# Kernel tuning notes

Measured on AMD Instinct MI355X. Metric: run time of the kernel, lower is better.

Reference implementation:

```python
import jax, jax.numpy as jnp
import numpy as np

B, N, T, D = 64, 76, 128, 128
AH, HEADS, DFF, FAH = 8, 4, 512, 128
DK = D // HEADS


def layer_norm(x, a, b, eps=1e-7):
    mean = x.mean(-1, keepdims=True)
    std = jnp.std(x, -1, ddof=1, keepdims=True)  # torch.std is unbiased
    return a * (x - mean) / (std + eps) + b


def setup_inputs() -> dict:
    key = jax.random.key(0)
    ks = jax.random.split(key, 32)
    w = lambda i, shape, s=0.05: (jax.random.normal(ks[i], shape, jnp.float32) * s)
    return {
        "H": jax.random.normal(ks[0], (B, N, T, D), jnp.float32),
        "mask": jax.random.randint(ks[1], (B, N, T), 0, 2).astype(jnp.float32),
        "feature_mask": jax.random.uniform(ks[2], (B, N), dtype=jnp.float32),
        # MissingAwareTemporalAttention params (shared across features)
        "Wt": w(3, (D, AH), 0.1), "Wx": w(4, (D, AH), 0.1),
        "rate": jnp.array([0.8], jnp.float32),
        "obs_bias": jnp.float32(0.5), "miss_bias": jnp.float32(0.0),
        # MultiHeadedAttention params (weights stored [in,out])
        "Wq": w(5, (D, D)), "bq": jnp.zeros(D, jnp.float32),
        "Wk": w(6, (D, D)), "bk": jnp.zeros(D, jnp.float32),
        "Wv": w(7, (D, D)), "bv": jnp.zeros(D, jnp.float32),
        "Wo": w(8, (D, D)), "bo": jnp.zeros(D, jnp.float32),
        # SublayerConnection LayerNorms
        "ln1_a": jnp.ones(D, jnp.float32), "ln1_b": jnp.zeros(D, jnp.float32),
        "ln2_a": jnp.ones(D, jnp.float32), "ln2_b": jnp.zeros(D, jnp.float32),
        # PositionwiseFeedForward
        "w1": w(9, (D, DFF)), "b1": jnp.zeros(DFF, jnp.float32),
        "w2": w(10, (DFF, D)), "b2": jnp.zeros(D, jnp.float32),
        # FinalAttentionQKV ('mul')
        "fWq": w(11, (D, FAH)), "fbq": jnp.zeros(FAH, jnp.float32),
        "fWk": w(12, (D, FAH)), "fbk": jnp.zeros(FAH, jnp.float32),
        "fWv": w(13, (D, FAH)), "fbv": jnp.zeros(FAH, jnp.float32),
        "mask_scale": jnp.float32(1.0),
    }


def concare_forward(H, mask, feature_mask, Wt, Wx, rate, obs_bias, miss_bias,
                    Wq, bq, Wk, bk, Wv, bv, Wo, bo, ln1_a, ln1_b, ln2_a, ln2_b,
                    w1, b1, w2, b2, fWq, fbq, fWk, fbk, fWv, fbv, mask_scale):
    # ---- MissingAwareTemporalAttention per feature (vectorized over N) ----
    q = jnp.einsum('bnd,da->bna', H[:, :, -1, :], Wt)           # [B,N,AH]
    k = jnp.einsum('bntd,da->bnta', H, Wx)                      # [B,N,T,AH]
    dot = jnp.einsum('bna,bnta->bnt', q, k)                     # [B,N,T]
    b_time = (jnp.arange(T - 1, -1, -1, dtype=jnp.float32) + 1.0)  # [T]
    sig = jax.nn.sigmoid(dot)
    denom = jax.nn.sigmoid(rate[0]) * (jnp.log(2.72 + (1.0 - sig)) * b_time)
    e = jax.nn.relu(sig / denom)
    e = e + jnp.where(mask > 0.5, obs_bias, miss_bias)
    a = jax.nn.softmax(e, axis=-1)                              # over T
    emb = jnp.einsum('bnt,bntd->bnd', a, H)                     # [B,N,D]

    # ---- SublayerConnection 1: pre-norm + MultiHeadedAttention + residual ----
    x0 = layer_norm(emb, ln1_a, ln1_b)
    qh = (x0 @ Wq + bq).reshape(B, N, HEADS, DK).transpose(0, 2, 1, 3)
    kh = (x0 @ Wk + bk).reshape(B, N, HEADS, DK).transpose(0, 2, 1, 3)
    vh = (x0 @ Wv + bv).reshape(B, N, HEADS, DK).transpose(0, 2, 1, 3)
    scores = jnp.einsum('bhqd,bhkd->bhqk', qh, kh) / np.sqrt(DK)
    p = jax.nn.softmax(scores, axis=-1)
    ctx = jnp.einsum('bhqk,bhkd->bhqd', p, vh).transpose(0, 2, 1, 3).reshape(B, N, D)
    mha = ctx @ Wo + bo                                          # [B,N,D]
    # DeCov regularizer over batch, per feature position
    feats = jnp.transpose(mha, (1, 2, 0))                        # [N,D,B]
    centered = feats - feats.mean(axis=2, keepdims=True)
    cov = jnp.einsum('ndb,neb->nde', centered, centered) / (B - 1)
    diag = jnp.einsum('ndd->nd', cov)
    decov = 0.5 * (jnp.sum(cov ** 2) - jnp.sum(diag ** 2))
    x = emb + mha

    # ---- SublayerConnection 2: pre-norm + FFN + residual ----
    x1 = layer_norm(x, ln2_a, ln2_b)
    ffn = jax.nn.relu(x1 @ w1 + b1) @ w2 + b2
    x = x + ffn                                                  # [B,N,D]

    # ---- FinalAttentionQKV ('mul') ----
    fq = x[:, -1, :] @ fWq + fbq                                 # [B,FAH]
    fk = x @ fWk + fbk                                           # [B,N,FAH]
    fv = x @ fWv + fbv                                           # [B,N,FAH]
    fe = jnp.einsum('bna,ba->bn', fk, fq)
    fe = fe + mask_scale * feature_mask
    alpha = jax.nn.softmax(fe, axis=1)                           # over N
    pooled = jnp.einsum('bn,bna->ba', alpha, fv)                 # [B,FAH]
    return pooled, decov


def reference(H, mask, feature_mask, Wt, Wx, rate, obs_bias, miss_bias,
              Wq, bq, Wk, bk, Wv, bv, Wo, bo, ln1_a, ln1_b, ln2_a, ln2_b,
              w1, b1, w2, b2, fWq, fbq, fWk, fbk, fWv, fbv, mask_scale):
    return concare_forward(H, mask, feature_mask, Wt, Wx, rate, obs_bias, miss_bias,
                           Wq, bq, Wk, bk, Wv, bv, Wo, bo, ln1_a, ln1_b, ln2_a, ln2_b,
                           w1, b1, w2, b2, fWq, fbq, fWk, fbk, fWv, fbv, mask_scale)
```

## Files before the change

kernel.cpp:

```cpp
#include <hip/hip_runtime.h>
#include <hip/hip_bf16.h>
#include <math.h>

#define BB 64
#define NN 76
#define TT 128
#define DD 128
#define AH 8
#define NHEADS 4
#define DFF 512
#define FAH 128
#define DK 32
#define BN (BB*NN)
#define ROWS 8
#define NBLK (BN/ROWS)

__device__ __forceinline__ void bar_lds() {
    asm volatile("s_waitcnt lgkmcnt(0)" ::: "memory");
    __builtin_amdgcn_s_barrier();
    __builtin_amdgcn_sched_barrier(0);
}

__global__ __launch_bounds__(512, 8) void k1_temporal(
    const float* __restrict__ H, const float* __restrict__ mask,
    const float* __restrict__ Wt, const float* __restrict__ Wx,
    const float* __restrict__ rate, const float* __restrict__ obs_bias,
    const float* __restrict__ miss_bias, float* __restrict__ emb)
{
    __shared__ __align__(16) float wtx[2*DD*AH];
    __shared__ __align__(16) float wqs[DD];
    __shared__ __align__(16) float dots[TT];
    __shared__ __align__(16) float as_[TT];
    __shared__ __align__(16) float parts[16][DD];
    __shared__ float qpart[2][AH];
    __shared__ float redsum[2];

    const int bid = blockIdx.x;
    const int tid = threadIdx.x;
    const size_t base = (size_t)bid * (TT*DD);
    const int lane = tid & 63, w = tid >> 6;
    const int c = tid & 31, g = tid >> 5;

    const float* wsrc = (tid < 256) ? (Wt + 4*tid) : (Wx + 4*(tid-256));
    const float4 wld = *(const float4*)wsrc;
    float r127 = 0.f, maskv = 0.f;
    if (tid < DD) {
        r127  = H[base + (TT-1)*DD + tid];
        maskv = mask[(size_t)bid*TT + tid];
    }
    const float sr   = 1.f / (1.f + expf(-rate[0]));
    const float obsv = obs_bias[0], missv = miss_bias[0];

    float4 h[8];
    const float4* Hg4 = (const float4*)(H + base);
    #pragma unroll
    for (int j = 0; j < 8; ++j) h[j] = Hg4[j*512 + tid];

    *(float4*)&wtx[4*tid] = wld;
    bar_lds();

    if (tid < DD) {
        float p[AH];
        #pragma unroll
        for (int a = 0; a < AH; ++a) p[a] = r127 * wtx[tid*AH + a];
        #pragma unroll
        for (int a = 0; a < AH; ++a) {
            float v = p[a];
            #pragma unroll
            for (int m = 1; m < 64; m <<= 1) v += __shfl_xor(v, m, 64);
            if (lane == 0) qpart[w][a] = v;
        }
    }
    bar_lds();
    if (tid < DD) {
        float acc = 0.f;
        #pragma unroll
        for (int a = 0; a < AH; ++a)
            acc += (qpart[0][a] + qpart[1][a]) * wtx[DD*AH + tid*AH + a];
        wqs[tid] = acc;
    }
    bar_lds();

    const float4 wq4 = *(const float4*)&wqs[4*c];
    #pragma unroll
    for (int j = 0; j < 8; ++j) {
        float p = h[j].x*wq4.x + h[j].y*wq4.y + h[j].z*wq4.z + h[j].w*wq4.w;
        #pragma unroll
        for (int m = 1; m < 32; m <<= 1) p += __shfl_xor(p, m, 64);
        if (c == 0) dots[g + 16*j] = p;
    }
    bar_lds();

    if (tid < TT) {
        const float dot = dots[tid];
        const float sig = 1.f / (1.f + expf(-dot));
        const float bt  = (float)(TT - tid);
        const float denom = sr * (logf(2.72f + (1.f - sig)) * bt);
        float e = fmaxf(sig / denom, 0.f);
        e += (maskv > 0.5f) ? obsv : missv;
        const float ex = expf(e);
        as_[tid] = ex;
        float vs = ex;
        #pragma unroll
        for (int m = 1; m < 64; m <<= 1) vs += __shfl_xor(vs, m, 64);
        if (lane == 0) redsum[w] = vs;
    }
    bar_lds();
    const float inv = 1.f / (redsum[0] + redsum[1]);

    float4 facc = make_float4(0.f, 0.f, 0.f, 0.f);
    #pragma unroll
    for (int j = 0; j < 8; ++j) {
        const float a = as_[g + 16*j];
        facc.x += a*h[j].x; facc.y += a*h[j].y;
        facc.z += a*h[j].z; facc.w += a*h[j].w;
    }
    *(float4*)&parts[g][4*c] = facc;
    bar_lds();
    if (tid < DD) {
        float acc = 0.f;
        #pragma unroll
        for (int gg = 0; gg < 16; ++gg) acc += parts[gg][tid];
        emb[(size_t)bid*DD + tid] = acc * inv;
    }
}

__global__ __launch_bounds__(256) void k2a_ln_qkv(
    const float* __restrict__ emb,
    const float* __restrict__ ln_a, const float* __restrict__ ln_b,
    const float* __restrict__ Wq, const float* __restrict__ bq,
    const float* __restrict__ Wk, const float* __restrict__ bk,
    const float* __restrict__ Wv, const float* __restrict__ bv,
    float* __restrict__ qb, float* __restrict__ kb, float* __restrict__ vb)
{
    __shared__ float xs[ROWS][DD];
    const int tid = threadIdx.x;
    const int r0 = blockIdx.x * ROWS;

    for (int i = tid; i < ROWS*DD; i += 256) {
        const int r = i / DD, d = i % DD;
        xs[r][d] = emb[(size_t)(r0+r)*DD + d];
    }
    __syncthreads();

    {
        const int wv_ = tid >> 6, lane = tid & 63;
        for (int rr = 0; rr < 2; ++rr) {
            const int r = wv_*2 + rr;
            const float x0 = xs[r][lane], x1 = xs[r][lane+64];
            float s = x0 + x1;
            #pragma unroll
            for (int m = 1; m < 64; m <<= 1) s += __shfl_xor(s, m, 64);
            const float mean = s / (float)DD;
            const float d0 = x0 - mean, d1 = x1 - mean;
            float v = d0*d0 + d1*d1;
            #pragma unroll
            for (int m = 1; m < 64; m <<= 1) v += __shfl_xor(v, m, 64);
            const float inv = 1.f / (sqrtf(v / (float)(DD-1)) + 1e-7f);
            xs[r][lane]    = ln_a[lane]   * (d0*inv) + ln_b[lane];
            xs[r][lane+64] = ln_a[lane+64]* (d1*inv) + ln_b[lane+64];
        }
    }
    __syncthreads();

    const int j = tid & 127, half = tid >> 7, rbase = half*4;
    float aq[4] = {0,0,0,0}, ak[4] = {0,0,0,0}, av[4] = {0,0,0,0};
    for (int d = 0; d < DD; ++d) {
        const float wqv = Wq[d*DD+j], wkv = Wk[d*DD+j], wvv = Wv[d*DD+j];
        #pragma unroll
        for (int r = 0; r < 4; ++r) {
            const float xv = xs[rbase+r][d];
            aq[r] += xv*wqv; ak[r] += xv*wkv; av[r] += xv*wvv;
        }
    }
    const float bqv = bq[j], bkv = bk[j], bvv = bv[j];
    #pragma unroll
    for (int r = 0; r < 4; ++r) {
        const size_t o = (size_t)(r0 + rbase + r)*DD + j;
        qb[o] = aq[r]+bqv; kb[o] = ak[r]+bkv; vb[o] = av[r]+bvv;
    }
}

__global__ __launch_bounds__(128) void k2b_attn(
    const float* __restrict__ qb, const float* __restrict__ kb,
    const float* __restrict__ vb, float* __restrict__ ctx)
{
    __shared__ float Qs[NN][DK], Ks[NN][DK], Vs[NN][DK];
    __shared__ float Ps[NN][NN+1];
    const int b = blockIdx.x / NHEADS, h = blockIdx.x % NHEADS;
    const int tid = threadIdx.x;
    const int co = h*DK;

    for (int i = tid; i < NN*DK; i += 128) {
        const int r = i / DK, c = i % DK;
        const size_t o = (size_t)(b*NN + r)*DD + co + c;
        Qs[r][c] = qb[o]; Ks[r][c] = kb[o]; Vs[r][c] = vb[o];
    }
    __syncthreads();

    const float scale = 0.17677669529663687f;
    if (tid < NN) {
        float qr[DK];
        #pragma unroll
        for (int c = 0; c < DK; ++c) qr[c] = Qs[tid][c];
        float mx = -1e30f;
        for (int k = 0; k < NN; ++k) {
            float s = 0.f;
            #pragma unroll
            for (int c = 0; c < DK; ++c) s += qr[c]*Ks[k][c];
            s *= scale;
            Ps[tid][k] = s;
            mx = fmaxf(mx, s);
        }
        float sum = 0.f;
        for (int k = 0; k < NN; ++k) { const float e = expf(Ps[tid][k]-mx); Ps[tid][k] = e; sum += e; }
        const float inv = 1.f/sum;
        float acc[DK];
        #pragma unroll
        for (int c = 0; c < DK; ++c) acc[c] = 0.f;
        for (int k = 0; k < NN; ++k) {
            const float p = Ps[tid][k];
            #pragma unroll
            for (int c = 0; c < DK; ++c) acc[c] += p*Vs[k][c];
        }
        const size_t o = (size_t)(b*NN + tid)*DD + co;
        #pragma unroll
        for (int c = 0; c < DK; ++c) ctx[o+c] = acc[c]*inv;
    }
}

__global__ __launch_bounds__(256) void k23_proj_ffn(
    const float* __restrict__ ctx, const float* __restrict__ emb,
    const float* __restrict__ Wo, const float* __restrict__ bo,
    const float* __restrict__ ln_a, const float* __restrict__ ln_b,
    const float* __restrict__ w1, const float* __restrict__ b1,
    const float* __restrict__ w2, const float* __restrict__ b2,
    float* __restrict__ mha, float* __restrict__ x2)
{
    __shared__ float cs[ROWS][DD];
    __shared__ float xs[ROWS][DD];
    __shared__ float x1s[ROWS][DD];
    __shared__ float hs[ROWS][DFF];
    __shared__ float parts[2][ROWS][DD];
    const int tid = threadIdx.x;
    const int r0 = blockIdx.x * ROWS;

    for (int i = tid; i < ROWS*DD; i += 256) {
        const int r = i / DD, d = i % DD;
        cs[r][d] = ctx[(size_t)(r0+r)*DD + d];
    }
    __syncthreads();

    {
        const int j = tid & 127, half = tid >> 7, rbase = half*4;
        float acc[4] = {0,0,0,0};
        for (int d = 0; d < DD; ++d) {
            const float wv = Wo[d*DD+j];
            #pragma unroll
            for (int r = 0; r < 4; ++r) acc[r] += cs[rbase+r][d]*wv;
        }
        const float bov = bo[j];
        #pragma unroll
        for (int r = 0; r < 4; ++r) {
            const size_t o = (size_t)(r0+rbase+r)*DD + j;
            const float m = acc[r] + bov;
            mha[o] = m;
            xs[rbase+r][j] = emb[o] + m;
        }
    }
    __syncthreads();

    {
        const int wv_ = tid >> 6, lane = tid & 63;
        for (int rr = 0; rr < 2; ++rr) {
            const int r = wv_*2 + rr;
            const float v0 = xs[r][lane], v1 = xs[r][lane+64];
            float s = v0 + v1;
            #pragma unroll
            for (int m = 1; m < 64; m <<= 1) s += __shfl_xor(s, m, 64);
            const float mean = s / (float)DD;
            const float d0 = v0-mean, d1 = v1-mean;
            float vv = d0*d0 + d1*d1;
            #pragma unroll
            for (int m = 1; m < 64; m <<= 1) vv += __shfl_xor(vv, m, 64);
            const float inv = 1.f / (sqrtf(vv/(float)(DD-1)) + 1e-7f);
            x1s[r][lane]    = ln_a[lane]   * (d0*inv) + ln_b[lane];
            x1s[r][lane+64] = ln_a[lane+64]* (d1*inv) + ln_b[lane+64];
        }
    }
    __syncthreads();

    {
        float acc0[ROWS], acc1[ROWS];
        #pragma unroll
        for (int r = 0; r < ROWS; ++r) { acc0[r]=0.f; acc1[r]=0.f; }
        for (int d = 0; d < DD; ++d) {
            const float wv0 = w1[d*DFF + tid], wv1 = w1[d*DFF + tid + 256];
            #pragma unroll
            for (int r = 0; r < ROWS; ++r) {
                const float xv = x1s[r][d];
                acc0[r] += xv*wv0; acc1[r] += xv*wv1;
            }
        }
        const float b10 = b1[tid], b11 = b1[tid+256];
        #pragma unroll
        for (int r = 0; r < ROWS; ++r) {
            hs[r][tid]     = fmaxf(acc0[r]+b10, 0.f);
            hs[r][tid+256] = fmaxf(acc1[r]+b11, 0.f);
        }
    }
    __syncthreads();

    {
        const int j = tid & 127, half = tid >> 7;
        float acc[ROWS];
        #pragma unroll
        for (int r = 0; r < ROWS; ++r) acc[r] = 0.f;
        for (int k = half*256; k < half*256 + 256; ++k) {
            const float wv = w2[k*DD + j];
            #pragma unroll
            for (int r = 0; r < ROWS; ++r) acc[r] += hs[r][k]*wv;
        }
        #pragma unroll
        for (int r = 0; r < ROWS; ++r) parts[half][r][j] = acc[r];
        __syncthreads();
        if (half == 0) {
            const float b2v = b2[j];
            #pragma unroll
            for (int r = 0; r < ROWS; ++r) {
                const size_t o = (size_t)(r0+r)*DD + j;
                x2[o] = xs[r][j] + parts[0][r][j] + parts[1][r][j] + b2v;
            }
        }
    }
}

__global__ __launch_bounds__(256) void k_decov(
    const float* __restrict__ mha, float* __restrict__ partial)
{
    __shared__ float Cs[BB][DD];
    __shared__ float means[DD];
    __shared__ float reda[256];
    __shared__ float redb[256];
    const int n = blockIdx.x, dc = blockIdx.y;
    const int tid = threadIdx.x;
    for (int i = tid; i < BB*DD; i += 256) {
        const int bb = i / DD, d = i % DD;
        Cs[bb][d] = mha[((size_t)bb*NN + n)*DD + d];
    }
    __syncthreads();
    if (tid < DD) {
        float s = 0.f;
        for (int bb = 0; bb < BB; ++bb) s += Cs[bb][tid];
        means[tid] = s / (float)BB;
    }
    __syncthreads();
    if (tid < DD) {
        const float m = means[tid];
        for (int bb = 0; bb < BB; ++bb) Cs[bb][tid] -= m;
    }
    __syncthreads();
    float ss = 0.f, dd2 = 0.f;
    const float invB1 = 1.f/63.f;
    for (int qi = tid; qi < 1024; qi += 256) {
        const int d  = dc*32 + qi / 32;
        const int e4 = (qi % 32) * 4;
        float a0=0,a1=0,a2=0,a3=0;
        for (int bb = 0; bb < BB; ++bb) {
            const float cd = Cs[bb][d];
            const float4 ce = *(const float4*)&Cs[bb][e4];
            a0 += cd*ce.x; a1 += cd*ce.y; a2 += cd*ce.z; a3 += cd*ce.w;
        }
        a0*=invB1; a1*=invB1; a2*=invB1; a3*=invB1;
        ss += a0*a0+a1*a1+a2*a2+a3*a3;
        if (d >= e4 && d < e4+4) {
            const float c[4] = {a0,a1,a2,a3};
            const float cd = c[d-e4];
            dd2 += cd*cd;
        }
    }
    reda[tid] = ss; redb[tid] = dd2;
    __syncthreads();
    for (int s2 = 128; s2 >= 1; s2 >>= 1) {
        if (tid < s2) { reda[tid] += reda[tid+s2]; redb[tid] += redb[tid+s2]; }
        __syncthreads();
    }
    if (tid == 0) partial[n*4 + dc] = 0.5f*(reda[0] - redb[0]);
}

__global__ __launch_bounds__(128) void k4_final(
    const float* __restrict__ x, const float* __restrict__ feature_mask,
    const float* __restrict__ fWq, const float* __restrict__ fbq,
    const float* __restrict__ fWk, const float* __restrict__ fbk,
    const float* __restrict__ fWv, const float* __restrict__ fbv,
    const float* __restrict__ mask_scale, const float* __restrict__ decov_partial,
    float* __restrict__ out)
{
    __shared__ float Xs[NN][DD];
    __shared__ float fqs[DD], gs[DD], ys[DD];
    __shared__ float es[NN];
    __shared__ float sc[2];
    const int b = blockIdx.x;
    const int tid = threadIdx.x;
    for (int i = tid; i < NN*DD; i += 128) {
        const int r = i / DD, d = i % DD;
        Xs[r][d] = x[((size_t)b*NN + r)*DD + d];
    }
    __syncthreads();
    {
        float acc = 0.f;
        for (int d = 0; d < DD; ++d) acc += Xs[NN-1][d] * fWq[d*FAH + tid];
        fqs[tid] = acc + fbq[tid];
    }
    __syncthreads();
    {
        float acc = 0.f;
        for (int a = 0; a < FAH; ++a) acc += fWk[tid*FAH + a] * fqs[a];
        gs[tid] = acc;
    }
    if (tid == 0) {
        float acc = 0.f;
        for (int a = 0; a < FAH; ++a) acc += fbk[a]*fqs[a];
        sc[0] = acc;
    }
    __syncthreads();
    const float msc = mask_scale[0];
    if (tid < NN) {
        float acc = 0.f;
        for (int d = 0; d < DD; ++d) acc += Xs[tid][d]*gs[d];
        es[tid] = acc + sc[0] + msc * feature_mask[b*NN + tid];
    }
    __syncthreads();
    if (tid == 0) {
        float mx = -1e30f;
        for (int n2 = 0; n2 < NN; ++n2) mx = fmaxf(mx, es[n2]);
        float sum = 0.f;
        for (int n2 = 0; n2 < NN; ++n2) { const float e = expf(es[n2]-mx); es[n2] = e; sum += e; }
        sc[1] = 1.f/sum;
    }
    __syncthreads();
    {
        const float inv = sc[1];
        float acc = 0.f;
        for (int n2 = 0; n2 < NN; ++n2) acc += es[n2]*Xs[n2][tid];
        ys[tid] = acc * inv;
    }
    __syncthreads();
    {
        float acc = 0.f;
        for (int d = 0; d < DD; ++d) acc += ys[d]*fWv[d*FAH + tid];
        out[(size_t)b*FAH + tid] = acc + fbv[tid];
    }
    if (b == 0 && tid == 0) {
        float s = 0.f;
        for (int i = 0; i < NN*4; ++i) s += decov_partial[i];
        out[BB*FAH] = s;
    }
}

extern "C" void kernel_launch(void* const* d_in, const int* in_sizes, int n_in,
                              void* d_out, int out_size, void* d_ws, size_t ws_size,
                              hipStream_t stream) {
    const float* H    = (const float*)d_in[0];
    const float* mask = (const float*)d_in[1];
    const float* fm   = (const float*)d_in[2];
    const float* Wt   = (const float*)d_in[3];
    const float* Wx   = (const float*)d_in[4];
    const float* rate = (const float*)d_in[5];
    const float* obs_bias  = (const float*)d_in[6];
    const float* miss_bias = (const float*)d_in[7];
    const float* Wq = (const float*)d_in[8];   const float* bq = (const float*)d_in[9];
    const float* Wk = (const float*)d_in[10];  const float* bk = (const float*)d_in[11];
    const float* Wv = (const float*)d_in[12];  const float* bv = (const float*)d_in[13];
    const float* Wo = (const float*)d_in[14];  const float* bo = (const float*)d_in[15];
    const float* ln1a = (const float*)d_in[16]; const float* ln1b = (const float*)d_in[17];
    const float* ln2a = (const float*)d_in[18]; const float* ln2b = (const float*)d_in[19];
    const float* w1 = (const float*)d_in[20];  const float* b1 = (const float*)d_in[21];
    const float* w2 = (const float*)d_in[22];  const float* b2 = (const float*)d_in[23];
    const float* fWq = (const float*)d_in[24]; const float* fbq = (const float*)d_in[25];
    const float* fWk = (const float*)d_in[26]; const float* fbk = (const float*)d_in[27];
    const float* fWv = (const float*)d_in[28]; const float* fbv = (const float*)d_in[29];
    const float* mask_scale = (const float*)d_in[30];
    float* out = (float*)d_out;

    float* ws = (float*)d_ws;
    const size_t S = (size_t)BN*DD;
    float* emb = ws;
    float* qb  = ws + 1*S;
    float* kb  = ws + 2*S;
    float* vb  = ws + 3*S;
    float* ctx = ws + 4*S;
    float* mha = ws + 5*S;
    float* x2  = ws + 6*S;
    float* dpart = ws + 7*S;

    k1_temporal<<<BN, 512, 0, stream>>>(H, mask, Wt, Wx, rate, obs_bias, miss_bias, emb);
    k2a_ln_qkv<<<NBLK, 256, 0, stream>>>(emb, ln1a, ln1b, Wq, bq, Wk, bk, Wv, bv, qb, kb, vb);
    k2b_attn<<<BB*NHEADS, 128, 0, stream>>>(qb, kb, vb, ctx);
    k23_proj_ffn<<<NBLK, 256, 0, stream>>>(ctx, emb, Wo, bo, ln2a, ln2b, w1, b1, w2, b2, mha, x2);
    k_decov<<<dim3(NN, 4), 256, 0, stream>>>(mha, dpart);
    k4_final<<<BB, 128, 0, stream>>>(x2, fm, fWq, fbq, fWk, fbk, fWv, fbv, mask_scale, dpart, out);
}
```

Baseline: 181.5 us.

## Double rows per block and merge decov and final attention into one launch

ROWS goes from 8 to 16 in the LN+QKV and projection+FFN kernels, so each block reuses every weight load across twice as many rows, at the cost of half as many blocks and more registers and LDS. The decov kernel and the final-attention kernel are merged into a single launch that branches on block index. Decov partials are now summed with atomicAdd into the output, which the projection kernel zeroes first. This removes one kernel launch and the serial partial-sum loop, but makes the floating-point summation order nondeterministic.

```diff
diff --git a/kernel.cpp b/kernel.cpp
--- a/kernel.cpp
+++ b/kernel.cpp
@@ -12,7 +12,7 @@
 #define FAH 128
 #define DK 32
 #define BN (BB*NN)
-#define ROWS 8
+#define ROWS 16
 #define NBLK (BN/ROWS)
 
 __device__ __forceinline__ void bar_lds() {
@@ -145,8 +145,8 @@
 
     {
         const int wv_ = tid >> 6, lane = tid & 63;
-        for (int rr = 0; rr < 2; ++rr) {
-            const int r = wv_*2 + rr;
+        for (int rr = 0; rr < 4; ++rr) {
+            const int r = wv_*4 + rr;
             const float x0 = xs[r][lane], x1 = xs[r][lane+64];
             float s = x0 + x1;
             #pragma unroll
@@ -163,19 +163,19 @@
     }
     __syncthreads();
 
-    const int j = tid & 127, half = tid >> 7, rbase = half*4;
-    float aq[4] = {0,0,0,0}, ak[4] = {0,0,0,0}, av[4] = {0,0,0,0};
+    const int j = tid & 127, half = tid >> 7, rbase = half*8;
+    float aq[8] = {0}, ak[8] = {0}, av[8] = {0};
     for (int d = 0; d < DD; ++d) {
         const float wqv = Wq[d*DD+j], wkv = Wk[d*DD+j], wvv = Wv[d*DD+j];
         #pragma unroll
-        for (int r = 0; r < 4; ++r) {
+        for (int r = 0; r < 8; ++r) {
             const float xv = xs[rbase+r][d];
             aq[r] += xv*wqv; ak[r] += xv*wkv; av[r] += xv*wvv;
         }
     }
     const float bqv = bq[j], bkv = bk[j], bvv = bv[j];
     #pragma unroll
-    for (int r = 0; r < 4; ++r) {
+    for (int r = 0; r < 8; ++r) {
         const size_t o = (size_t)(r0 + rbase + r)*DD + j;
         qb[o] = aq[r]+bqv; kb[o] = ak[r]+bkv; vb[o] = av[r]+bvv;
     }
@@ -235,7 +235,7 @@
     const float* __restrict__ ln_a, const float* __restrict__ ln_b,
     const float* __restrict__ w1, const float* __restrict__ b1,
     const float* __restrict__ w2, const float* __restrict__ b2,
-    float* __restrict__ mha, float* __restrict__ x2)
+    float* __restrict__ mha, float* __restrict__ x2, float* __restrict__ out)
 {
     __shared__ float cs[ROWS][DD];
     __shared__ float xs[ROWS][DD];
@@ -245,6 +245,8 @@
     const int tid = threadIdx.x;
     const int r0 = blockIdx.x * ROWS;
 
+    if (blockIdx.x == 0 && tid == 0) out[BB*FAH] = 0.f;
+
     for (int i = tid; i < ROWS*DD; i += 256) {
         const int r = i / DD, d = i % DD;
         cs[r][d] = ctx[(size_t)(r0+r)*DD + d];
@@ -252,16 +254,16 @@
     __syncthreads();
 
     {
-        const int j = tid & 127, half = tid >> 7, rbase = half*4;
-        float acc[4] = {0,0,0,0};
+        const int j = tid & 127, half = tid >> 7, rbase = half*8;
+        float acc[8] = {0};
         for (int d = 0; d < DD; ++d) {
             const float wv = Wo[d*DD+j];
             #pragma unroll
-            for (int r = 0; r < 4; ++r) acc[r] += cs[rbase+r][d]*wv;
+            for (int r = 0; r < 8; ++r) acc[r] += cs[rbase+r][d]*wv;
         }
         const float bov = bo[j];
         #pragma unroll
-        for (int r = 0; r < 4; ++r) {
+        for (int r = 0; r < 8; ++r) {
             const size_t o = (size_t)(r0+rbase+r)*DD + j;
             const float m = acc[r] + bov;
             mha[o] = m;
@@ -272,8 +274,8 @@
 
     {
         const int wv_ = tid >> 6, lane = tid & 63;
-        for (int rr = 0; rr < 2; ++rr) {
-            const int r = wv_*2 + rr;
+        for (int rr = 0; rr < 4; ++rr) {
+            const int r = wv_*4 + rr;
             const float v0 = xs[r][lane], v1 = xs[r][lane+64];
             float s = v0 + v1;
             #pragma unroll
@@ -335,85 +337,84 @@
     }
 }
 
-__global__ __launch_bounds__(256) void k_decov(
-    const float* __restrict__ mha, float* __restrict__ partial)
-{
-    __shared__ float Cs[BB][DD];
-    __shared__ float means[DD];
-    __shared__ float reda[256];
-    __shared__ float redb[256];
-    const int n = blockIdx.x, dc = blockIdx.y;
-    const int tid = threadIdx.x;
-    for (int i = tid; i < BB*DD; i += 256) {
-        const int bb = i / DD, d = i % DD;
-        Cs[bb][d] = mha[((size_t)bb*NN + n)*DD + d];
-    }
-    __syncthreads();
-    if (tid < DD) {
-        float s = 0.f;
-        for (int bb = 0; bb < BB; ++bb) s += Cs[bb][tid];
-        means[tid] = s / (float)BB;
-    }
-    __syncthreads();
-    if (tid < DD) {
-        const float m = means[tid];
-        for (int bb = 0; bb < BB; ++bb) Cs[bb][tid] -= m;
-    }
-    __syncthreads();
-    float ss = 0.f, dd2 = 0.f;
-    const float invB1 = 1.f/63.f;
-    for (int qi = tid; qi < 1024; qi += 256) {
-        const int d  = dc*32 + qi / 32;
-        const int e4 = (qi % 32) * 4;
-        float a0=0,a1=0,a2=0,a3=0;
-        for (int bb = 0; bb < BB; ++bb) {
-            const float cd = Cs[bb][d];
-            const float4 ce = *(const float4*)&Cs[bb][e4];
-            a0 += cd*ce.x; a1 += cd*ce.y; a2 += cd*ce.z; a3 += cd*ce.w;
-        }
-        a0*=invB1; a1*=invB1; a2*=invB1; a3*=invB1;
-        ss += a0*a0+a1*a1+a2*a2+a3*a3;
-        if (d >= e4 && d < e4+4) {
-            const float c[4] = {a0,a1,a2,a3};
-            const float cd = c[d-e4];
-            dd2 += cd*cd;
-        }
-    }
-    reda[tid] = ss; redb[tid] = dd2;
-    __syncthreads();
-    for (int s2 = 128; s2 >= 1; s2 >>= 1) {
-        if (tid < s2) { reda[tid] += reda[tid+s2]; redb[tid] += redb[tid+s2]; }
-        __syncthreads();
-    }
-    if (tid == 0) partial[n*4 + dc] = 0.5f*(reda[0] - redb[0]);
-}
-
-__global__ __launch_bounds__(128) void k4_final(
-    const float* __restrict__ x, const float* __restrict__ feature_mask,
+__global__ __launch_bounds__(256) void k_final(
+    const float* __restrict__ mha, const float* __restrict__ x,
+    const float* __restrict__ feature_mask,
     const float* __restrict__ fWq, const float* __restrict__ fbq,
     const float* __restrict__ fWk, const float* __restrict__ fbk,
     const float* __restrict__ fWv, const float* __restrict__ fbv,
-    const float* __restrict__ mask_scale, const float* __restrict__ decov_partial,
-    float* __restrict__ out)
+    const float* __restrict__ mask_scale, float* __restrict__ out)
 {
+    const int tid = threadIdx.x;
+
+    if (blockIdx.x < NN*4) {
+        __shared__ float Cs[BB][DD];
+        __shared__ float means[DD];
+        __shared__ float reda[256];
+        __shared__ float redb[256];
+        const int n = blockIdx.x >> 2, dc = blockIdx.x & 3;
+        for (int i = tid; i < BB*DD; i += 256) {
+            const int bb = i / DD, d = i % DD;
+            Cs[bb][d] = mha[((size_t)bb*NN + n)*DD + d];
+        }
+        __syncthreads();
+        if (tid < DD) {
+            float s = 0.f;
+            for (int bb = 0; bb < BB; ++bb) s += Cs[bb][tid];
+            means[tid] = s / (float)BB;
+        }
+        __syncthreads();
+        if (tid < DD) {
+            const float m = means[tid];
+            for (int bb = 0; bb < BB; ++bb) Cs[bb][tid] -= m;
+        }
+        __syncthreads();
+        float ss = 0.f, dd2 = 0.f;
+        const float invB1 = 1.f/63.f;
+        for (int qi = tid; qi < 1024; qi += 256) {
+            const int d  = dc*32 + qi / 32;
+            const int e4 = (qi % 32) * 4;
+            float a0=0,a1=0,a2=0,a3=0;
+            for (int bb = 0; bb < BB; ++bb) {
+                const float cd = Cs[bb][d];
+                const float4 ce = *(const float4*)&Cs[bb][e4];
+                a0 += cd*ce.x; a1 += cd*ce.y; a2 += cd*ce.z; a3 += cd*ce.w;
+            }
+            a0*=invB1; a1*=invB1; a2*=invB1; a3*=invB1;
+            ss += a0*a0+a1*a1+a2*a2+a3*a3;
+            if (d >= e4 && d < e4+4) {
+                const float c[4] = {a0,a1,a2,a3};
+                const float cd = c[d-e4];
+                dd2 += cd*cd;
+            }
+        }
+        reda[tid] = ss; redb[tid] = dd2;
+        __syncthreads();
+        for (int s2 = 128; s2 >= 1; s2 >>= 1) {
+            if (tid < s2) { reda[tid] += reda[tid+s2]; redb[tid] += redb[tid+s2]; }
+            __syncthreads();
+        }
+        if (tid == 0) atomicAdd(&out[BB*FAH], 0.5f*(reda[0] - redb[0]));
+        return;
+    }
+
     __shared__ float Xs[NN][DD];
     __shared__ float fqs[DD], gs[DD], ys[DD];
     __shared__ float es[NN];
     __shared__ float sc[2];
-    const int b = blockIdx.x;
-    const int tid = threadIdx.x;
-    for (int i = tid; i < NN*DD; i += 128) {
+    const int b = blockIdx.x - NN*4;
+    for (int i = tid; i < NN*DD; i += 256) {
         const int r = i / DD, d = i % DD;
         Xs[r][d] = x[((size_t)b*NN + r)*DD + d];
     }
     __syncthreads();
-    {
+    if (tid < FAH) {
         float acc = 0.f;
         for (int d = 0; d < DD; ++d) acc += Xs[NN-1][d] * fWq[d*FAH + tid];
         fqs[tid] = acc + fbq[tid];
     }
     __syncthreads();
-    {
+    if (tid < DD) {
         float acc = 0.f;
         for (int a = 0; a < FAH; ++a) acc += fWk[tid*FAH + a] * fqs[a];
         gs[tid] = acc;
@@ -439,22 +440,17 @@
         sc[1] = 1.f/sum;
     }
     __syncthreads();
-    {
+    if (tid < DD) {
         const float inv = sc[1];
         float acc = 0.f;
         for (int n2 = 0; n2 < NN; ++n2) acc += es[n2]*Xs[n2][tid];
         ys[tid] = acc * inv;
     }
     __syncthreads();
-    {
+    if (tid < FAH) {
         float acc = 0.f;
         for (int d = 0; d < DD; ++d) acc += ys[d]*fWv[d*FAH + tid];
         out[(size_t)b*FAH + tid] = acc + fbv[tid];
-    }
-    if (b == 0 && tid == 0) {
-        float s = 0.f;
-        for (int i = 0; i < NN*4; ++i) s += decov_partial[i];
-        out[BB*FAH] = s;
     }
 }
 
@@ -492,12 +488,10 @@
     float* ctx = ws + 4*S;
     float* mha = ws + 5*S;
     float* x2  = ws + 6*S;
-    float* dpart = ws + 7*S;
 
     k1_temporal<<<BN, 512, 0, stream>>>(H, mask, Wt, Wx, rate, obs_bias, miss_bias, emb);
     k2a_ln_qkv<<<NBLK, 256, 0, stream>>>(emb, ln1a, ln1b, Wq, bq, Wk, bk, Wv, bv, qb, kb, vb);
     k2b_attn<<<BB*NHEADS, 128, 0, stream>>>(qb, kb, vb, ctx);
-    k23_proj_ffn<<<NBLK, 256, 0, stream>>>(ctx, emb, Wo, bo, ln2a, ln2b, w1, b1, w2, b2, mha, x2);
-    k_decov<<<dim3(NN, 4), 256, 0, stream>>>(mha, dpart);
-    k4_final<<<BB, 128, 0, stream>>>(x2, fm, fWq, fbq, fWk, fbk, fWv, fbv, mask_scale, dpart, out);
-}
+    k23_proj_ffn<<<NBLK, 256, 0, stream>>>(ctx, emb, Wo, bo, ln2a, ln2b, w1, b1, w2, b2, mha, x2, out);
+    k_final<<<NN*4 + BB, 256, 0, stream>>>(mha, x2, fm, fWq, fbq, fWk, fbk, fWv, fbv, mask_scale, out);
+}
```

After: 225.2 us. 24.1% more time.

## Compute query projection and softmax redundantly per wave to cut block barriers

Applied to the files above, without the earlier changes.

The temporal attention kernel now has every wave compute the query projection and the attention softmax weights itself, using shuffles and padded LDS weight layouts, instead of a few threads computing them and sharing through shared memory. This removes three block-wide barriers and the shared-memory staging of intermediate values. In exchange each wave repeats the same transcendental and reduction work, and the occupancy hint in launch bounds drops from 8 to 6.

```diff
diff --git a/kernel.cpp b/kernel.cpp
--- a/kernel.cpp
+++ b/kernel.cpp
@@ -21,24 +21,23 @@
     __builtin_amdgcn_sched_barrier(0);
 }
 
-__global__ __launch_bounds__(512, 8) void k1_temporal(
+__global__ __launch_bounds__(512, 6) void k1_temporal(
     const float* __restrict__ H, const float* __restrict__ mask,
     const float* __restrict__ Wt, const float* __restrict__ Wx,
     const float* __restrict__ rate, const float* __restrict__ obs_bias,
     const float* __restrict__ miss_bias, float* __restrict__ emb)
 {
-    __shared__ __align__(16) float wtx[2*DD*AH];
-    __shared__ __align__(16) float wqs[DD];
+    __shared__ __align__(16) float wts[DD*9];
+    __shared__ __align__(16) float wxp[DD*10];
+    __shared__ __align__(16) float r127s[DD];
+    __shared__ __align__(16) float masks[DD];
     __shared__ __align__(16) float dots[TT];
-    __shared__ __align__(16) float as_[TT];
     __shared__ __align__(16) float parts[16][DD];
-    __shared__ float qpart[2][AH];
-    __shared__ float redsum[2];
 
     const int bid = blockIdx.x;
     const int tid = threadIdx.x;
     const size_t base = (size_t)bid * (TT*DD);
-    const int lane = tid & 63, w = tid >> 6;
+    const int lane = tid & 63;
     const int c = tid & 31, g = tid >> 5;
 
     const float* wsrc = (tid < 256) ? (Wt + 4*tid) : (Wx + 4*(tid-256));
@@ -56,32 +55,35 @@
     #pragma unroll
     for (int j = 0; j < 8; ++j) h[j] = Hg4[j*512 + tid];
 
-    *(float4*)&wtx[4*tid] = wld;
+    {
+        const int lin0 = 4 * ((tid < 256) ? tid : (tid - 256));
+        const float v[4] = {wld.x, wld.y, wld.z, wld.w};
+        #pragma unroll
+        for (int k = 0; k < 4; ++k) {
+            const int lin = lin0 + k;
+            const int d = lin >> 3, a = lin & 7;
+            if (tid < 256) wts[d*9 + a] = v[k];
+            else           wxp[d*10 + a] = v[k];
+        }
+    }
+    if (tid < DD) { r127s[tid] = r127; masks[tid] = maskv; }
     bar_lds();
 
-    if (tid < DD) {
-        float p[AH];
-        #pragma unroll
-        for (int a = 0; a < AH; ++a) p[a] = r127 * wtx[tid*AH + a];
+    float4 wq4 = make_float4(0.f, 0.f, 0.f, 0.f);
+    {
+        const float r0 = r127s[lane], r1 = r127s[lane + 64];
         #pragma unroll
         for (int a = 0; a < AH; ++a) {
-            float v = p[a];
+            float v = r0 * wts[lane*9 + a] + r1 * wts[(lane+64)*9 + a];
             #pragma unroll
             for (int m = 1; m < 64; m <<= 1) v += __shfl_xor(v, m, 64);
-            if (lane == 0) qpart[w][a] = v;
-        }
-    }
-    bar_lds();
-    if (tid < DD) {
-        float acc = 0.f;
-        #pragma unroll
-        for (int a = 0; a < AH; ++a)
-            acc += (qpart[0][a] + qpart[1][a]) * wtx[DD*AH + tid*AH + a];
-        wqs[tid] = acc;
-    }
-    bar_lds();
-
-    const float4 wq4 = *(const float4*)&wqs[4*c];
+            wq4.x += v * wxp[(4*c+0)*10 + a];
+            wq4.y += v * wxp[(4*c+1)*10 + a];
+            wq4.z += v * wxp[(4*c+2)*10 + a];
+            wq4.w += v * wxp[(4*c+3)*10 + a];
+        }
+    }
+
     #pragma unroll
     for (int j = 0; j < 8; ++j) {
         float p = h[j].x*wq4.x + h[j].y*wq4.y + h[j].z*wq4.z + h[j].w*wq4.w;
@@ -91,37 +93,42 @@
     }
     bar_lds();
 
-    if (tid < TT) {
-        const float dot = dots[tid];
-        const float sig = 1.f / (1.f + expf(-dot));
-        const float bt  = (float)(TT - tid);
-        const float denom = sr * (logf(2.72f + (1.f - sig)) * bt);
-        float e = fmaxf(sig / denom, 0.f);
-        e += (maskv > 0.5f) ? obsv : missv;
-        const float ex = expf(e);
-        as_[tid] = ex;
-        float vs = ex;
-        #pragma unroll
-        for (int m = 1; m < 64; m <<= 1) vs += __shfl_xor(vs, m, 64);
-        if (lane == 0) redsum[w] = vs;
-    }
-    bar_lds();
-    const float inv = 1.f / (redsum[0] + redsum[1]);
+    float ex0, ex1;
+    {
+        const float d0 = dots[lane],      m0 = masks[lane];
+        const float d1 = dots[lane + 64], m1 = masks[lane + 64];
+        const float sig0 = 1.f / (1.f + expf(-d0));
+        const float sig1 = 1.f / (1.f + expf(-d1));
+        const float bt0 = (float)(TT - lane);
+        const float bt1 = (float)(TT - (lane + 64));
+        float e0 = fmaxf(sig0 / (sr * (logf(2.72f + (1.f - sig0)) * bt0)), 0.f);
+        float e1 = fmaxf(sig1 / (sr * (logf(2.72f + (1.f - sig1)) * bt1)), 0.f);
+        e0 += (m0 > 0.5f) ? obsv : missv;
+        e1 += (m1 > 0.5f) ? obsv : missv;
+        ex0 = expf(e0);
+        ex1 = expf(e1);
+    }
+    float vs = ex0 + ex1;
+    #pragma unroll
+    for (int m = 1; m < 64; m <<= 1) vs += __shfl_xor(vs, m, 64);
+    const float inv = 1.f / vs;
 
     float4 facc = make_float4(0.f, 0.f, 0.f, 0.f);
     #pragma unroll
     for (int j = 0; j < 8; ++j) {
-        const float a = as_[g + 16*j];
+        const int src = g + 16 * (j & 3);
+        const float a = (j < 4) ? __shfl(ex0, src, 64) : __shfl(ex1, src, 64);
         facc.x += a*h[j].x; facc.y += a*h[j].y;
         facc.z += a*h[j].z; facc.w += a*h[j].w;
     }
+    facc.x *= inv; facc.y *= inv; facc.z *= inv; facc.w *= inv;
     *(float4*)&parts[g][4*c] = facc;
     bar_lds();
     if (tid < DD) {
         float acc = 0.f;
         #pragma unroll
         for (int gg = 0; gg < 16; ++gg) acc += parts[gg][tid];
-        emb[(size_t)bid*DD + tid] = acc * inv;
+        emb[(size_t)bid*DD + tid] = acc;
     }
 }
 
```

New measurement: 185.7 us. 2.3% more time.
